# Kernel optimization log

Hardware: AMD Instinct MI355X
Metric: run time of the kernel (lower is better)

## Reference

```python
import jax, jax.numpy as jnp
import numpy as np

V, T_BLOCK, D, H, L, HS = 32000, 1024, 1024, 16, 6, 64
B, T = 4, 1024
EPS = 1e-5


def setup_inputs() -> dict:
    key = jax.random.key(0)
    ks = jax.random.split(key, 12)
    s = 0.02  # init std, matches _init_weights
    return {
        'input_tokens': jax.random.randint(ks[0], (B, T), 0, V),
        'tok_emb': jax.random.normal(ks[1], (V, D), jnp.float32) * s,
        'pos_emb': jax.random.normal(ks[2], (T_BLOCK, D), jnp.float32) * s,
        'Wq': jax.random.normal(ks[3], (L, H, D, HS), jnp.float32) * s,
        'Wk': jax.random.normal(ks[4], (L, H, D, HS), jnp.float32) * s,
        'Wv': jax.random.normal(ks[5], (L, H, D, HS), jnp.float32) * s,
        'Wo': jax.random.normal(ks[6], (L, D, D), jnp.float32) * s,
        'bo': jnp.zeros((L, D), jnp.float32),
        'ln1_g': jnp.ones((L, D), jnp.float32),
        'ln1_b': jnp.zeros((L, D), jnp.float32),
        'ln2_g': jnp.ones((L, D), jnp.float32),
        'ln2_b': jnp.zeros((L, D), jnp.float32),
        'W1': jax.random.normal(ks[7], (L, D, 4 * D), jnp.float32) * s,
        'b1': jnp.zeros((L, 4 * D), jnp.float32),
        'W2': jax.random.normal(ks[8], (L, 4 * D, D), jnp.float32) * s,
        'b2': jnp.zeros((L, D), jnp.float32),
        'lnf_g': jnp.ones((D,), jnp.float32),
        'lnf_b': jnp.zeros((D,), jnp.float32),
        'W_out': jax.random.normal(ks[9], (D, V), jnp.float32) * s,
        'b_out': jnp.zeros((V,), jnp.float32),
    }


def _layer_norm(x, g, b):
    mu = jnp.mean(x, axis=-1, keepdims=True)
    var = jnp.mean(jnp.square(x - mu), axis=-1, keepdims=True)
    return (x - mu) * jax.lax.rsqrt(var + EPS) * g + b


def _attn(x, Wq, Wk, Wv, Wo, bo, causal_mask):
    # x: [B,T,D]; Wq/Wk/Wv: [H,D,hs] (per-head linears, bias=False)
    q = jnp.einsum('btd,hds->bhts', x, Wq)
    k = jnp.einsum('btd,hds->bhts', x, Wk)
    v = jnp.einsum('btd,hds->bhts', x, Wv)
    scores = jnp.einsum('bhts,bhus->bhtu', q, k) * (HS ** -0.5)
    scores = jnp.where(causal_mask, scores, -jnp.inf)
    w = jax.nn.softmax(scores, axis=-1)  # dropout=0.0 -> identity
    o = jnp.einsum('bhtu,bhus->bhts', w, v)
    # concat heads in order, then projection
    o = o.transpose(0, 2, 1, 3).reshape(x.shape[0], x.shape[1], H * HS)
    return o @ Wo + bo


def reference(input_tokens, tok_emb, pos_emb, Wq, Wk, Wv, Wo, bo,
              ln1_g, ln1_b, ln2_g, ln2_b, W1, b1, W2, b2,
              lnf_g, lnf_b, W_out, b_out):
    Bc, Tc = input_tokens.shape
    x = tok_emb[input_tokens] + pos_emb[:Tc]  # [B,T,D]
    mask = jnp.tril(jnp.ones((Tc, Tc), bool))[None, None]  # [1,1,T,T]
    for l in range(L):
        x = x + _attn(_layer_norm(x, ln1_g[l], ln1_b[l]),
                      Wq[l], Wk[l], Wv[l], Wo[l], bo[l], mask)
        h = _layer_norm(x, ln2_g[l], ln2_b[l])
        x = x + jax.nn.relu(h @ W1[l] + b1[l]) @ W2[l] + b2[l]
    x = _layer_norm(x, lnf_g, lnf_b)
    logits = x @ W_out + b_out  # [B,T,V]
    return logits
```

## Files before the change

### kernel.cpp

```cpp
#include <hip/hip_runtime.h>
#include <hip/hip_bf16.h>

#define HS 64
#define NH 16
#define DMODEL 1024
#define SEQ 1024
#define NB 4
#define NL 6
#define VOCAB 32000
#define EPS_LN 1e-5f

static constexpr int ROWS = NB * SEQ;

typedef float f32x4 __attribute__((ext_vector_type(4)));
typedef short bf16x8 __attribute__((ext_vector_type(8)));
typedef unsigned short u16x8 __attribute__((ext_vector_type(8)));
typedef unsigned short u16x4 __attribute__((ext_vector_type(4)));

__device__ __forceinline__ unsigned short f2b(float f) {
  __hip_bfloat16 h = __float2bfloat16(f);
  return *reinterpret_cast<unsigned short*>(&h);
}
__device__ __forceinline__ void gload_lds16(const void* g, void* l) {
  __builtin_amdgcn_global_load_lds(
      (const __attribute__((address_space(1))) void*)g,
      (__attribute__((address_space(3))) void*)l, 16, 0, 0);
}
#define MFMA16 __builtin_amdgcn_mfma_f32_16x16x32_bf16

__global__ __launch_bounds__(256) void embed_kernel(
    const int* __restrict__ tokens, const float* __restrict__ tok_emb,
    const float* __restrict__ pos_emb, float* __restrict__ x) {
  int row = blockIdx.x;
  int t = row & (SEQ - 1);
  int tok = tokens[row];
  int d = threadIdx.x * 4;
  float4 te = *(const float4*)(tok_emb + (size_t)tok * DMODEL + d);
  float4 pe = *(const float4*)(pos_emb + (size_t)t * DMODEL + d);
  te.x += pe.x; te.y += pe.y; te.z += pe.z; te.w += pe.w;
  *(float4*)(x + (size_t)row * DMODEL + d) = te;
}

__global__ __launch_bounds__(256) void ln_kernel(
    const float* __restrict__ in, unsigned short* __restrict__ outp,
    const float* __restrict__ g, const float* __restrict__ b) {
  int row = blockIdx.x;
  int tid = threadIdx.x;
  const float* xr = in + (size_t)row * DMODEL;
  float4 v4 = *(const float4*)(xr + tid * 4);
  float s = v4.x + v4.y + v4.z + v4.w;
  float s2 = v4.x * v4.x + v4.y * v4.y + v4.z * v4.z + v4.w * v4.w;
#pragma unroll
  for (int off = 32; off > 0; off >>= 1) {
    s  += __shfl_down(s, off, 64);
    s2 += __shfl_down(s2, off, 64);
  }
  __shared__ float red[8];
  __shared__ float stats[2];
  int wv = tid >> 6, lane = tid & 63;
  if (lane == 0) { red[wv] = s; red[4 + wv] = s2; }
  __syncthreads();
  if (tid == 0) {
    float ts = red[0] + red[1] + red[2] + red[3];
    float ts2 = red[4] + red[5] + red[6] + red[7];
    float mu = ts * (1.0f / DMODEL);
    float var = ts2 * (1.0f / DMODEL) - mu * mu;
    stats[0] = mu;
    stats[1] = rsqrtf(var + EPS_LN);
  }
  __syncthreads();
  float mu = stats[0], rstd = stats[1];
  float4 g4 = *(const float4*)(g + tid * 4);
  float4 b4 = *(const float4*)(b + tid * 4);
  u16x4 o;
  o[0] = f2b((v4.x - mu) * rstd * g4.x + b4.x);
  o[1] = f2b((v4.y - mu) * rstd * g4.y + b4.y);
  o[2] = f2b((v4.z - mu) * rstd * g4.z + b4.z);
  o[3] = f2b((v4.w - mu) * rstd * g4.w + b4.w);
  *(u16x4*)(outp + (size_t)row * DMODEL + tid * 4) = o;
}

__global__ __launch_bounds__(256) void transconv(
    const float* __restrict__ in, unsigned short* __restrict__ outp, int K, int N) {
  __shared__ float tile[32][33];
  size_t zoff = (size_t)blockIdx.z * K * N;
  in += zoff;
  outp += zoff;
  int n0 = blockIdx.x * 32, k0 = blockIdx.y * 32;
  int tx = threadIdx.x & 31, ty = threadIdx.x >> 5;
#pragma unroll
  for (int i = 0; i < 4; ++i)
    tile[ty + i * 8][tx] = in[(size_t)(k0 + ty + i * 8) * N + n0 + tx];
  __syncthreads();
#pragma unroll
  for (int i = 0; i < 4; ++i)
    outp[(size_t)(n0 + ty + i * 8) * K + k0 + tx] = f2b(tile[tx][ty + i * 8]);
}

__global__ __launch_bounds__(256) void qkv_transconv(
    const float* __restrict__ Wq, const float* __restrict__ Wk,
    const float* __restrict__ Wv, unsigned short* __restrict__ outp) {
  __shared__ float tile[32][33];
  int z = blockIdx.z;
  int l = z / 48;
  int r = z % 48;
  int which = r >> 4, h = r & 15;
  const float* W = (which == 0 ? Wq : which == 1 ? Wk : Wv) +
                   ((size_t)l * NH + h) * DMODEL * HS;
  int d0 = blockIdx.y * 32, s0 = blockIdx.x * 32;
  int tx = threadIdx.x & 31, ty = threadIdx.x >> 5;
#pragma unroll
  for (int i = 0; i < 4; ++i)
    tile[ty + i * 8][tx] = W[(size_t)(d0 + ty + i * 8) * HS + s0 + tx];
  __syncthreads();
  unsigned short* ob = outp + ((size_t)l * 3072 + which * 1024 + h * 64) * DMODEL;
#pragma unroll
  for (int i = 0; i < 4; ++i)
    ob[(size_t)(s0 + ty + i * 8) * DMODEL + d0 + tx] = f2b(tile[tx][ty + i * 8]);
}

#define EPI_LOGITS 0
#define EPI_RES 1
#define EPI_RELU 2
#define EPI_QKV 3

template <int EPI, int BM_>
__global__ __launch_bounds__(512, 2) void mmX(
    const unsigned short* __restrict__ A, const unsigned short* __restrict__ Bt,
    const float* __restrict__ bias, const float* __restrict__ res,
    float* __restrict__ outf, unsigned short* __restrict__ ob0,
    unsigned short* __restrict__ ob1, unsigned short* __restrict__ ob2,
    int M, int N, int K) {
  constexpr int NA = BM_ / 64;
  constexpr int AP = BM_ / 128;
  constexpr int MFRAG = BM_ / 32;
  __shared__ __align__(16) unsigned short LDS[2][(BM_ + 256) * 64];
  const int tid = threadIdx.x;
  const int lane = tid & 63, w = tid >> 6;
  const int wm2 = w >> 2, wn4 = w & 3;
  const int l15 = lane & 15, l4 = lane >> 4;

  const int nM = M / BM_, nN = N >> 8;
  const int nwg = nM * nN;
  int bid = blockIdx.x;
  int wg = (bid & 7) * (nwg >> 3) + (bid >> 3);
  int mb = wg % nM, nb = wg / nM;
  const int m0 = mb * BM_, n0 = nb * 256;

  const int srow = tid >> 3;
  const int scolb = (tid & 7) * 16;
  const int swst = (srow & 7) << 4;
  const char* aS = (const char*)A + ((size_t)(m0 + srow) * K) * 2 + (scolb ^ swst);
  const char* bS = (const char*)Bt + ((size_t)(n0 + srow) * K) * 2 + (scolb ^ swst);
  const size_t rstep = (size_t)64 * K * 2;

  const int kb0 = l4 * 16;
  const int swz = (l15 & 7) << 4;

  const int NT = K >> 6;
  f32x4 acc[MFRAG][4] = {};
  bf16x8 bv[4][2], avA[AP][2], avB[AP][2];

#define STAGEX(tt)                                                          \
  {                                                                         \
    unsigned short* ad = &LDS[(tt) & 1][0] + (size_t)tid * 8;               \
    unsigned short* bd = &LDS[(tt) & 1][BM_ * 64] + (size_t)tid * 8;        \
    size_t ko = (size_t)(tt) * 128;                                         \
    _Pragma("unroll")                                                       \
    for (int j = 0; j < NA; ++j) gload_lds16(aS + ko + j * rstep, ad + j * 4096); \
    _Pragma("unroll")                                                       \
    for (int j = 0; j < 4; ++j) gload_lds16(bS + ko + j * rstep, bd + j * 4096);  \
  }

#define READA(dst, p)                                                       \
  _Pragma("unroll")                                                         \
  for (int mm = 0; mm < AP; ++mm)                                           \
  _Pragma("unroll")                                                         \
    for (int ks = 0; ks < 2; ++ks)                                          \
      dst[mm][ks] = *(const bf16x8*)(ab + (AP * (p) + mm) * 2048 +          \
                                     ((kb0 + 64 * ks) ^ swz));

#define GROUP(src, p)                                                       \
  __builtin_amdgcn_s_setprio(1);                                            \
  _Pragma("unroll")                                                         \
  for (int ks = 0; ks < 2; ++ks)                                            \
  _Pragma("unroll")                                                         \
    for (int mm = 0; mm < AP; ++mm)                                         \
    _Pragma("unroll")                                                       \
      for (int ni = 0; ni < 4; ++ni)                                        \
        acc[AP * (p) + mm][ni] =                                            \
            MFMA16(src[mm][ks], bv[ni][ks], acc[AP * (p) + mm][ni], 0, 0, 0);\
  __builtin_amdgcn_s_setprio(0);

  STAGEX(0)
  STAGEX(1)

  for (int t = 0; t < NT; ++t) {
    if (t < NT - 1) {
      if constexpr (BM_ == 256) asm volatile("s_waitcnt vmcnt(8)" ::: "memory");
      else                      asm volatile("s_waitcnt vmcnt(6)" ::: "memory");
    } else {
      asm volatile("s_waitcnt vmcnt(0)" ::: "memory");
    }
    __builtin_amdgcn_s_barrier();
    __builtin_amdgcn_sched_barrier(0);
    const char* ab = (const char*)&LDS[t & 1][0] +
                     (size_t)(wm2 * (BM_ / 2) + l15) * 128;
    const char* bb = (const char*)&LDS[t & 1][BM_ * 64] +
                     (size_t)(wn4 * 64 + l15) * 128;
#pragma unroll
    for (int ni = 0; ni < 4; ++ni)
#pragma unroll
      for (int ks = 0; ks < 2; ++ks)
        bv[ni][ks] = *(const bf16x8*)(bb + ni * 2048 + ((kb0 + 64 * ks) ^ swz));
    READA(avA, 0)
    READA(avB, 1)
    GROUP(avA, 0)
    READA(avA, 2)
    GROUP(avB, 1)
    READA(avB, 3)
    GROUP(avA, 2)
    asm volatile("s_waitcnt lgkmcnt(0)" ::: "memory");
    __builtin_amdgcn_sched_barrier(0);
    __builtin_amdgcn_s_barrier();
    __builtin_amdgcn_sched_barrier(0);
    if (t + 2 < NT) STAGEX(t + 2)
    GROUP(avB, 3)
  }
#undef STAGEX
#undef READA
#undef GROUP

  int rbase = m0 + wm2 * (BM_ / 2) + (l4 << 2);
  int cbase = n0 + wn4 * 64 + l15;
#pragma unroll
  for (int ni = 0; ni < 4; ++ni) {
    int col = cbase + ni * 16;
    float bvv = 0.f;
    if (EPI != EPI_QKV) bvv = bias[col];
    if (EPI == EPI_QKV) {
      int which = col >> 10;
      int c2 = col & 1023;
      int h = c2 >> 6, s = c2 & 63;
#pragma unroll
      for (int mi = 0; mi < MFRAG; ++mi) {
        f32x4 a4 = acc[mi][ni];
        int row0 = rbase + mi * 16;
        int bb2 = row0 >> 10, t0 = row0 & 1023;
        if (which == 2) {
          u16x4 pk;
          pk[0] = f2b(a4[0]); pk[1] = f2b(a4[1]); pk[2] = f2b(a4[2]); pk[3] = f2b(a4[3]);
          *(u16x4*)(ob2 + ((((size_t)bb2 * NH + h) * HS) + s) * SEQ + t0) = pk;
        } else {
          unsigned short* dst = (which == 0) ? ob0 : ob1;
#pragma unroll
          for (int r = 0; r < 4; ++r)
            dst[((((size_t)bb2 * NH) + h) * SEQ + t0 + r) * HS + s] = f2b(a4[r]);
        }
      }
    } else {
#pragma unroll
      for (int mi = 0; mi < MFRAG; ++mi) {
        f32x4 a4 = acc[mi][ni];
#pragma unroll
        for (int r = 0; r < 4; ++r) {
          int rowg = rbase + mi * 16 + r;
          size_t off = (size_t)rowg * N + col;
          float v = a4[r] + bvv;
          if (EPI == EPI_RES) outf[off] = v + res[off];
          else if (EPI == EPI_LOGITS) outf[off] = v;
          else if (EPI == EPI_RELU) ob0[off] = f2b(fmaxf(v, 0.f));
        }
      }
    }
  }
}

__global__ __launch_bounds__(256) void attn_mfma(
    const unsigned short* __restrict__ q, const unsigned short* __restrict__ k,
    const unsigned short* __restrict__ vt, unsigned short* __restrict__ outp) {
  __shared__ __align__(16) unsigned short S[8192];
  unsigned short* Ks = S;
  unsigned short* Vs = S + 4096;
  int qt = blockIdx.x, bh = blockIdx.y;
  int tid = threadIdx.x;
  int lane = tid & 63, w = tid >> 6;
  int l15 = lane & 15, l4 = lane >> 4;

  const unsigned short* qb = q + (size_t)bh * SEQ * HS;
  const unsigned short* kb = k + (size_t)bh * SEQ * HS;
  const unsigned short* vb = vt + (size_t)bh * HS * SEQ;

  int q_l = w * 16 + l15;
  int q_g = qt * 64 + q_l;
  bf16x8 qf[2];
  qf[0] = *(const bf16x8*)(qb + (size_t)q_g * HS + l4 * 8);
  qf[1] = *(const bf16x8*)(qb + (size_t)q_g * HS + l4 * 8 + 32);

  int i0 = tid, i1 = tid + 256;
  int kOff0 = (i0 >> 7) * 16 * HS + (i0 & 15) * HS + ((i0 >> 4) & 7) * 8;
  int kOff1 = (i1 >> 7) * 16 * HS + (i1 & 15) * HS + ((i1 >> 4) & 7) * 8;
  int vOff0 = ((i0 >> 7) * 16 + (i0 & 15)) * SEQ + ((i0 >> 4) & 7) * 8;
  int vOff1 = ((i1 >> 7) * 16 + (i1 & 15)) * SEQ + ((i1 >> 4) & 7) * 8;

  f32x4 o[4] = {};
  float mrun = -1e30f, lrun = 0.f;
  int baseLane = 32 * (l4 & 1) + l15;
  bool hi_t = (l4 >> 1) != 0;

  for (int kt = 0; kt <= qt; ++kt) {
    __syncthreads();
    const unsigned short* ksrc = kb + (size_t)kt * 64 * HS;
    gload_lds16(ksrc + kOff0, Ks + (size_t)i0 * 8);
    gload_lds16(ksrc + kOff1, Ks + (size_t)i1 * 8);
    gload_lds16(vb + vOff0 + kt * 64, Vs + (size_t)i0 * 8);
    gload_lds16(vb + vOff1 + kt * 64, Vs + (size_t)i1 * 8);
    __syncthreads();

    f32x4 s[4];
#pragma unroll
    for (int t = 0; t < 4; ++t) {
      bf16x8 kf0 = *(const bf16x8*)(Ks + ((size_t)(t * 8 + l4) * 16 + l15) * 8);
      bf16x8 kf1 = *(const bf16x8*)(Ks + ((size_t)(t * 8 + l4 + 4) * 16 + l15) * 8);
      s[t] = (f32x4){0.f, 0.f, 0.f, 0.f};
      s[t] = MFMA16(kf0, qf[0], s[t], 0, 0, 0);
      s[t] = MFMA16(kf1, qf[1], s[t], 0, 0, 0);
    }

    bool diag = (kt == qt);
    int keybase = kt * 64 + 4 * l4;
    float mx = -1e30f;
#pragma unroll
    for (int t = 0; t < 4; ++t)
#pragma unroll
      for (int r = 0; r < 4; ++r) {
        float sv = s[t][r] * 0.125f;
        if (diag && (keybase + 16 * t + r) > q_g) sv = -1e30f;
        s[t][r] = sv;
        mx = fmaxf(mx, sv);
      }
    mx = fmaxf(mx, __shfl_xor(mx, 16, 64));
    mx = fmaxf(mx, __shfl_xor(mx, 32, 64));
    float mnew = fmaxf(mrun, mx);
    float sc = __expf(mrun - mnew);
    float ps = 0.f;
    float p[4][4];
#pragma unroll
    for (int t = 0; t < 4; ++t)
#pragma unroll
      for (int r = 0; r < 4; ++r) {
        float e = __expf(s[t][r] - mnew);
        p[t][r] = e;
        ps += e;
      }
    ps += __shfl_xor(ps, 16, 64);
    ps += __shfl_xor(ps, 32, 64);
    lrun = lrun * sc + ps;
    mrun = mnew;
#pragma unroll
    for (int t2 = 0; t2 < 4; ++t2)
#pragma unroll
      for (int r = 0; r < 4; ++r) o[t2][r] *= sc;

    int pd[4][2];
#pragma unroll
    for (int t = 0; t < 4; ++t)
#pragma unroll
      for (int h = 0; h < 2; ++h)
        pd[t][h] = (int)f2b(p[t][2 * h]) | ((int)f2b(p[t][2 * h + 1]) << 16);

#pragma unroll
    for (int kk = 0; kk < 2; ++kk) {
      int a0 = __shfl(pd[2 * kk][0], baseLane, 64);
      int b0 = __shfl(pd[2 * kk + 1][0], baseLane, 64);
      int a1 = __shfl(pd[2 * kk][1], baseLane, 64);
      int b1 = __shfl(pd[2 * kk + 1][1], baseLane, 64);
      int a2 = __shfl(pd[2 * kk][0], baseLane + 16, 64);
      int b2 = __shfl(pd[2 * kk + 1][0], baseLane + 16, 64);
      int a3 = __shfl(pd[2 * kk][1], baseLane + 16, 64);
      int b3 = __shfl(pd[2 * kk + 1][1], baseLane + 16, 64);
      union { int4 i4; bf16x8 v; } yu;
      yu.i4.x = hi_t ? b0 : a0;
      yu.i4.y = hi_t ? b1 : a1;
      yu.i4.z = hi_t ? b2 : a2;
      yu.i4.w = hi_t ? b3 : a3;
#pragma unroll
      for (int t2 = 0; t2 < 4; ++t2) {
        bf16x8 vf = *(const bf16x8*)(Vs + ((size_t)(t2 * 8 + l4 + 4 * kk) * 16 + l15) * 8);
        o[t2] = MFMA16(vf, yu.v, o[t2], 0, 0, 0);
      }
    }
  }

  __syncthreads();
  float inv = 1.0f / lrun;
  unsigned short* Ol = S;
#pragma unroll
  for (int t2 = 0; t2 < 4; ++t2) {
    u16x4 p4;
#pragma unroll
    for (int r = 0; r < 4; ++r) p4[r] = f2b(o[t2][r] * inv);
    *(u16x4*)(Ol + (size_t)q_l * 72 + 16 * t2 + 4 * l4) = p4;
  }
  __syncthreads();
  int row = tid >> 2, hs0 = (tid & 3) * 16;
  int bidx = bh >> 4, h = bh & 15;
  size_t gbase = ((size_t)bidx * SEQ + qt * 64 + row) * DMODEL + h * HS + hs0;
  u16x8 r0 = *(const u16x8*)(Ol + (size_t)row * 72 + hs0);
  u16x8 r1 = *(const u16x8*)(Ol + (size_t)row * 72 + hs0 + 8);
  *(u16x8*)(outp + gbase) = r0;
  *(u16x8*)(outp + gbase + 8) = r1;
}

extern "C" void kernel_launch(void* const* d_in, const int* in_sizes, int n_in,
                              void* d_out, int out_size, void* d_ws, size_t ws_size,
                              hipStream_t stream) {
  const int*   tokens  = (const int*)d_in[0];
  const float* tok_emb = (const float*)d_in[1];
  const float* pos_emb = (const float*)d_in[2];
  const float* Wq      = (const float*)d_in[3];
  const float* Wk      = (const float*)d_in[4];
  const float* Wv      = (const float*)d_in[5];
  const float* Wo      = (const float*)d_in[6];
  const float* bo      = (const float*)d_in[7];
  const float* ln1_g   = (const float*)d_in[8];
  const float* ln1_b   = (const float*)d_in[9];
  const float* ln2_g   = (const float*)d_in[10];
  const float* ln2_b   = (const float*)d_in[11];
  const float* W1      = (const float*)d_in[12];
  const float* b1      = (const float*)d_in[13];
  const float* W2      = (const float*)d_in[14];
  const float* b2      = (const float*)d_in[15];
  const float* lnf_g   = (const float*)d_in[16];
  const float* lnf_b   = (const float*)d_in[17];
  const float* W_out   = (const float*)d_in[18];
  const float* b_out   = (const float*)d_in[19];
  float* logits = (float*)d_out;

  char* p = (char*)d_ws;
  float* x = (float*)p;            p += (size_t)ROWS * DMODEL * 4;
  unsigned short* hb = (unsigned short*)p;  p += (size_t)ROWS * DMODEL * 2;
  unsigned short* qb = (unsigned short*)p;  p += (size_t)ROWS * DMODEL * 2;
  unsigned short* kb = (unsigned short*)p;  p += (size_t)ROWS * DMODEL * 2;
  unsigned short* vtb = (unsigned short*)p; p += (size_t)ROWS * DMODEL * 2;
  unsigned short* att = (unsigned short*)p; p += (size_t)ROWS * DMODEL * 2;
  unsigned short* hid = (unsigned short*)p; p += (size_t)ROWS * 4 * DMODEL * 2;
  unsigned short* qkvt = (unsigned short*)p; p += (size_t)NL * 3 * DMODEL * DMODEL * 2;
  unsigned short* wot = (unsigned short*)p;  p += (size_t)NL * DMODEL * DMODEL * 2;
  unsigned short* w1t = (unsigned short*)p;  p += (size_t)NL * 4 * DMODEL * DMODEL * 2;
  unsigned short* w2t = (unsigned short*)p;  p += (size_t)NL * 4 * DMODEL * DMODEL * 2;
  unsigned short* woutt = (unsigned short*)p; p += (size_t)VOCAB * DMODEL * 2;

  transconv<<<dim3(32, 32, NL), 256, 0, stream>>>(Wo, wot, DMODEL, DMODEL);
  transconv<<<dim3(128, 32, NL), 256, 0, stream>>>(W1, w1t, DMODEL, 4 * DMODEL);
  transconv<<<dim3(32, 128, NL), 256, 0, stream>>>(W2, w2t, 4 * DMODEL, DMODEL);
  transconv<<<dim3(1000, 32, 1), 256, 0, stream>>>(W_out, woutt, DMODEL, VOCAB);
  qkv_transconv<<<dim3(2, 32, NL * 48), 256, 0, stream>>>(Wq, Wk, Wv, qkvt);

  embed_kernel<<<ROWS, 256, 0, stream>>>(tokens, tok_emb, pos_emb, x);

  for (int l = 0; l < NL; ++l) {
    ln_kernel<<<ROWS, 256, 0, stream>>>(x, hb, ln1_g + l * DMODEL, ln1_b + l * DMODEL);
    mmX<EPI_QKV, 256><<<192, 512, 0, stream>>>(
        hb, qkvt + (size_t)l * 3 * DMODEL * DMODEL, nullptr, nullptr,
        nullptr, qb, kb, vtb, ROWS, 3 * DMODEL, DMODEL);
    attn_mfma<<<dim3(SEQ / 64, NB * NH), 256, 0, stream>>>(qb, kb, vtb, att);
    mmX<EPI_RES, 128><<<128, 512, 0, stream>>>(
        att, wot + (size_t)l * DMODEL * DMODEL, bo + l * DMODEL, x,
        x, nullptr, nullptr, nullptr, ROWS, DMODEL, DMODEL);
    ln_kernel<<<ROWS, 256, 0, stream>>>(x, hb, ln2_g + l * DMODEL, ln2_b + l * DMODEL);
    mmX<EPI_RELU, 256><<<256, 512, 0, stream>>>(
        hb, w1t + (size_t)l * 4 * DMODEL * DMODEL, b1 + (size_t)l * 4 * DMODEL, nullptr,
        nullptr, hid, nullptr, nullptr, ROWS, 4 * DMODEL, DMODEL);
    mmX<EPI_RES, 128><<<128, 512, 0, stream>>>(
        hid, w2t + (size_t)l * 4 * DMODEL * DMODEL, b2 + l * DMODEL, x,
        x, nullptr, nullptr, nullptr, ROWS, DMODEL, 4 * DMODEL);
  }

  ln_kernel<<<ROWS, 256, 0, stream>>>(x, hb, lnf_g, lnf_b);
  mmX<EPI_LOGITS, 256><<<2000, 512, 0, stream>>>(
      hb, woutt, b_out, nullptr, logits, nullptr, nullptr, nullptr,
      ROWS, VOCAB, DMODEL);
}
```

Before: 1.942 ms.

## Vectorize weight transposes, stage logits via LDS, double-buffer attention with lazy rescale

The transpose kernels now handle 64x32 tiles and write eight bf16 values per thread as one 16-byte store, replacing scattered 2-byte stores. The logits GEMM epilogue stages each accumulator half through LDS so it can issue coalesced nontemporal float4 stores to the large logits buffer. The attention kernel double-buffers K/V tiles so the next tile loads while the current one computes, and uses exp2 with a prescaled constant. It also skips the online-softmax rescale unless the running max grows past a threshold. These changes add LDS use and sync points in the GEMM epilogue, and the lazy rescale lets intermediate values grow up to 2^8 before renormalizing.

```diff
diff --git a/kernel.cpp b/kernel.cpp
--- a/kernel.cpp
+++ b/kernel.cpp
@@ -27,6 +27,7 @@
       (__attribute__((address_space(3))) void*)l, 16, 0, 0);
 }
 #define MFMA16 __builtin_amdgcn_mfma_f32_16x16x32_bf16
+#define EXP2F __builtin_amdgcn_exp2f
 
 __global__ __launch_bounds__(256) void embed_kernel(
     const int* __restrict__ tokens, const float* __restrict__ tok_emb,
@@ -82,41 +83,47 @@
 
 __global__ __launch_bounds__(256) void transconv(
     const float* __restrict__ in, unsigned short* __restrict__ outp, int K, int N) {
-  __shared__ float tile[32][33];
+  __shared__ float tile[64][33];
   size_t zoff = (size_t)blockIdx.z * K * N;
   in += zoff;
   outp += zoff;
-  int n0 = blockIdx.x * 32, k0 = blockIdx.y * 32;
+  int n0 = blockIdx.x * 32, k0 = blockIdx.y * 64;
   int tx = threadIdx.x & 31, ty = threadIdx.x >> 5;
 #pragma unroll
-  for (int i = 0; i < 4; ++i)
+  for (int i = 0; i < 8; ++i)
     tile[ty + i * 8][tx] = in[(size_t)(k0 + ty + i * 8) * N + n0 + tx];
   __syncthreads();
-#pragma unroll
-  for (int i = 0; i < 4; ++i)
-    outp[(size_t)(n0 + ty + i * 8) * K + k0 + tx] = f2b(tile[tx][ty + i * 8]);
+  int n = threadIdx.x >> 3;
+  int kq = (threadIdx.x & 7) * 8;
+  u16x8 o8;
+#pragma unroll
+  for (int j = 0; j < 8; ++j) o8[j] = f2b(tile[kq + j][n]);
+  *(u16x8*)(outp + (size_t)(n0 + n) * K + k0 + kq) = o8;
 }
 
 __global__ __launch_bounds__(256) void qkv_transconv(
     const float* __restrict__ Wq, const float* __restrict__ Wk,
     const float* __restrict__ Wv, unsigned short* __restrict__ outp) {
-  __shared__ float tile[32][33];
+  __shared__ float tile[64][33];
   int z = blockIdx.z;
   int l = z / 48;
   int r = z % 48;
   int which = r >> 4, h = r & 15;
   const float* W = (which == 0 ? Wq : which == 1 ? Wk : Wv) +
                    ((size_t)l * NH + h) * DMODEL * HS;
-  int d0 = blockIdx.y * 32, s0 = blockIdx.x * 32;
+  int s0 = blockIdx.x * 32, d0 = blockIdx.y * 64;
   int tx = threadIdx.x & 31, ty = threadIdx.x >> 5;
 #pragma unroll
-  for (int i = 0; i < 4; ++i)
+  for (int i = 0; i < 8; ++i)
     tile[ty + i * 8][tx] = W[(size_t)(d0 + ty + i * 8) * HS + s0 + tx];
   __syncthreads();
   unsigned short* ob = outp + ((size_t)l * 3072 + which * 1024 + h * 64) * DMODEL;
-#pragma unroll
-  for (int i = 0; i < 4; ++i)
-    ob[(size_t)(s0 + ty + i * 8) * DMODEL + d0 + tx] = f2b(tile[tx][ty + i * 8]);
+  int n = threadIdx.x >> 3;
+  int kq = (threadIdx.x & 7) * 8;
+  u16x8 o8;
+#pragma unroll
+  for (int j = 0; j < 8; ++j) o8[j] = f2b(tile[kq + j][n]);
+  *(u16x8*)(ob + (size_t)(s0 + n) * DMODEL + d0 + kq) = o8;
 }
 
 #define EPI_LOGITS 0
@@ -233,43 +240,75 @@
 
   int rbase = m0 + wm2 * (BM_ / 2) + (l4 << 2);
   int cbase = n0 + wn4 * 64 + l15;
-#pragma unroll
-  for (int ni = 0; ni < 4; ++ni) {
-    int col = cbase + ni * 16;
-    float bvv = 0.f;
-    if (EPI != EPI_QKV) bvv = bias[col];
-    if (EPI == EPI_QKV) {
-      int which = col >> 10;
-      int c2 = col & 1023;
-      int h = c2 >> 6, s = c2 & 63;
-#pragma unroll
-      for (int mi = 0; mi < MFRAG; ++mi) {
-        f32x4 a4 = acc[mi][ni];
-        int row0 = rbase + mi * 16;
-        int bb2 = row0 >> 10, t0 = row0 & 1023;
-        if (which == 2) {
-          u16x4 pk;
-          pk[0] = f2b(a4[0]); pk[1] = f2b(a4[1]); pk[2] = f2b(a4[2]); pk[3] = f2b(a4[3]);
-          *(u16x4*)(ob2 + ((((size_t)bb2 * NH + h) * HS) + s) * SEQ + t0) = pk;
-        } else {
-          unsigned short* dst = (which == 0) ? ob0 : ob1;
-#pragma unroll
-          for (int r = 0; r < 4; ++r)
-            dst[((((size_t)bb2 * NH) + h) * SEQ + t0 + r) * HS + s] = f2b(a4[r]);
+
+  if constexpr (EPI == EPI_LOGITS) {
+    float* fl = (float*)&LDS[0][0];
+#pragma unroll
+    for (int half = 0; half < 2; ++half) {
+      __syncthreads();
+      if (wm2 == half) {
+#pragma unroll
+        for (int ni = 0; ni < 4; ++ni) {
+          float bvv = bias[cbase + ni * 16];
+          int cl = wn4 * 64 + l15 + ni * 16;
+#pragma unroll
+          for (int mi = 0; mi < MFRAG; ++mi) {
+            int rl = mi * 16 + (l4 << 2);
+#pragma unroll
+            for (int r = 0; r < 4; ++r)
+              fl[(rl + r) * 256 + cl] = acc[mi][ni][r] + bvv;
+          }
         }
       }
-    } else {
-#pragma unroll
-      for (int mi = 0; mi < MFRAG; ++mi) {
-        f32x4 a4 = acc[mi][ni];
-#pragma unroll
-        for (int r = 0; r < 4; ++r) {
-          int rowg = rbase + mi * 16 + r;
-          size_t off = (size_t)rowg * N + col;
-          float v = a4[r] + bvv;
-          if (EPI == EPI_RES) outf[off] = v + res[off];
-          else if (EPI == EPI_LOGITS) outf[off] = v;
-          else if (EPI == EPI_RELU) ob0[off] = f2b(fmaxf(v, 0.f));
+      __syncthreads();
+#pragma unroll
+      for (int j = 0; j < 16; ++j) {
+        int idx = j * 512 + tid;
+        int rl = idx >> 6;
+        int cc = (idx & 63) << 2;
+        f32x4 v4 = *(const f32x4*)&fl[rl * 256 + cc];
+        float* gp = outf + (size_t)(m0 + half * 128 + rl) * N + n0 + cc;
+        __builtin_nontemporal_store(v4, (f32x4*)gp);
+      }
+    }
+  } else {
+#pragma unroll
+    for (int ni = 0; ni < 4; ++ni) {
+      int col = cbase + ni * 16;
+      float bvv = 0.f;
+      if (EPI != EPI_QKV) bvv = bias[col];
+      if (EPI == EPI_QKV) {
+        int which = col >> 10;
+        int c2 = col & 1023;
+        int h = c2 >> 6, s = c2 & 63;
+#pragma unroll
+        for (int mi = 0; mi < MFRAG; ++mi) {
+          f32x4 a4 = acc[mi][ni];
+          int row0 = rbase + mi * 16;
+          int bb2 = row0 >> 10, t0 = row0 & 1023;
+          if (which == 2) {
+            u16x4 pk;
+            pk[0] = f2b(a4[0]); pk[1] = f2b(a4[1]); pk[2] = f2b(a4[2]); pk[3] = f2b(a4[3]);
+            *(u16x4*)(ob2 + ((((size_t)bb2 * NH + h) * HS) + s) * SEQ + t0) = pk;
+          } else {
+            unsigned short* dst = (which == 0) ? ob0 : ob1;
+#pragma unroll
+            for (int r = 0; r < 4; ++r)
+              dst[((((size_t)bb2 * NH) + h) * SEQ + t0 + r) * HS + s] = f2b(a4[r]);
+          }
+        }
+      } else {
+#pragma unroll
+        for (int mi = 0; mi < MFRAG; ++mi) {
+          f32x4 a4 = acc[mi][ni];
+#pragma unroll
+          for (int r = 0; r < 4; ++r) {
+            int rowg = rbase + mi * 16 + r;
+            size_t off = (size_t)rowg * N + col;
+            float v = a4[r] + bvv;
+            if (EPI == EPI_RES) outf[off] = v + res[off];
+            else if (EPI == EPI_RELU) ob0[off] = f2b(fmaxf(v, 0.f));
+          }
         }
       }
     }
@@ -279,9 +318,9 @@
 __global__ __launch_bounds__(256) void attn_mfma(
     const unsigned short* __restrict__ q, const unsigned short* __restrict__ k,
     const unsigned short* __restrict__ vt, unsigned short* __restrict__ outp) {
-  __shared__ __align__(16) unsigned short S[8192];
+  __shared__ __align__(16) unsigned short S[16384];
   unsigned short* Ks = S;
-  unsigned short* Vs = S + 4096;
+  unsigned short* Vs = S + 8192;
   int qt = blockIdx.x, bh = blockIdx.y;
   int tid = threadIdx.x;
   int lane = tid & 63, w = tid >> 6;
@@ -303,64 +342,82 @@
   int vOff0 = ((i0 >> 7) * 16 + (i0 & 15)) * SEQ + ((i0 >> 4) & 7) * 8;
   int vOff1 = ((i1 >> 7) * 16 + (i1 & 15)) * SEQ + ((i1 >> 4) & 7) * 8;
 
+#define ASTAGE(tt)                                                           \
+  {                                                                          \
+    int bsel = ((tt) & 1) * 4096;                                            \
+    const unsigned short* ksrc = kb + (size_t)(tt) * 64 * HS;                \
+    gload_lds16(ksrc + kOff0, Ks + bsel + (size_t)i0 * 8);                   \
+    gload_lds16(ksrc + kOff1, Ks + bsel + (size_t)i1 * 8);                   \
+    gload_lds16(vb + vOff0 + (tt) * 64, Vs + bsel + (size_t)i0 * 8);         \
+    gload_lds16(vb + vOff1 + (tt) * 64, Vs + bsel + (size_t)i1 * 8);         \
+  }
+
   f32x4 o[4] = {};
-  float mrun = -1e30f, lrun = 0.f;
+  float mrun = -3e38f, lrun = 0.f;
   int baseLane = 32 * (l4 & 1) + l15;
   bool hi_t = (l4 >> 1) != 0;
+  const float CSC = 0.125f * 1.44269504f;
+  const float THR = 8.0f / CSC;
+
+  ASTAGE(0)
 
   for (int kt = 0; kt <= qt; ++kt) {
-    __syncthreads();
-    const unsigned short* ksrc = kb + (size_t)kt * 64 * HS;
-    gload_lds16(ksrc + kOff0, Ks + (size_t)i0 * 8);
-    gload_lds16(ksrc + kOff1, Ks + (size_t)i1 * 8);
-    gload_lds16(vb + vOff0 + kt * 64, Vs + (size_t)i0 * 8);
-    gload_lds16(vb + vOff1 + kt * 64, Vs + (size_t)i1 * 8);
-    __syncthreads();
+    asm volatile("s_waitcnt vmcnt(0)" ::: "memory");
+    __builtin_amdgcn_s_barrier();
+    __builtin_amdgcn_sched_barrier(0);
+    if (kt < qt) ASTAGE(kt + 1)
+    const unsigned short* Kb = Ks + (kt & 1) * 4096;
+    const unsigned short* Vb = Vs + (kt & 1) * 4096;
 
     f32x4 s[4];
 #pragma unroll
     for (int t = 0; t < 4; ++t) {
-      bf16x8 kf0 = *(const bf16x8*)(Ks + ((size_t)(t * 8 + l4) * 16 + l15) * 8);
-      bf16x8 kf1 = *(const bf16x8*)(Ks + ((size_t)(t * 8 + l4 + 4) * 16 + l15) * 8);
+      bf16x8 kf0 = *(const bf16x8*)(Kb + ((size_t)(t * 8 + l4) * 16 + l15) * 8);
+      bf16x8 kf1 = *(const bf16x8*)(Kb + ((size_t)(t * 8 + l4 + 4) * 16 + l15) * 8);
       s[t] = (f32x4){0.f, 0.f, 0.f, 0.f};
       s[t] = MFMA16(kf0, qf[0], s[t], 0, 0, 0);
       s[t] = MFMA16(kf1, qf[1], s[t], 0, 0, 0);
     }
 
-    bool diag = (kt == qt);
-    int keybase = kt * 64 + 4 * l4;
-    float mx = -1e30f;
+    if (kt == qt) {
+      int keybase = kt * 64 + 4 * l4;
+#pragma unroll
+      for (int t = 0; t < 4; ++t)
+#pragma unroll
+        for (int r = 0; r < 4; ++r)
+          if (keybase + 16 * t + r > q_g) s[t][r] = -3e38f;
+    }
+    float mx = -3e38f;
 #pragma unroll
     for (int t = 0; t < 4; ++t)
 #pragma unroll
-      for (int r = 0; r < 4; ++r) {
-        float sv = s[t][r] * 0.125f;
-        if (diag && (keybase + 16 * t + r) > q_g) sv = -1e30f;
-        s[t][r] = sv;
-        mx = fmaxf(mx, sv);
-      }
+      for (int r = 0; r < 4; ++r) mx = fmaxf(mx, s[t][r]);
     mx = fmaxf(mx, __shfl_xor(mx, 16, 64));
     mx = fmaxf(mx, __shfl_xor(mx, 32, 64));
-    float mnew = fmaxf(mrun, mx);
-    float sc = __expf(mrun - mnew);
+    if (!__all(mx - mrun <= THR)) {
+      float mnew = fmaxf(mrun, mx);
+      float sc = EXP2F((mrun - mnew) * CSC);
+      lrun *= sc;
+#pragma unroll
+      for (int t2 = 0; t2 < 4; ++t2)
+#pragma unroll
+        for (int r = 0; r < 4; ++r) o[t2][r] *= sc;
+      mrun = mnew;
+    }
+    float mc = mrun * CSC;
     float ps = 0.f;
     float p[4][4];
 #pragma unroll
     for (int t = 0; t < 4; ++t)
 #pragma unroll
       for (int r = 0; r < 4; ++r) {
-        float e = __expf(s[t][r] - mnew);
+        float e = EXP2F(__builtin_fmaf(s[t][r], CSC, -mc));
         p[t][r] = e;
         ps += e;
       }
     ps += __shfl_xor(ps, 16, 64);
     ps += __shfl_xor(ps, 32, 64);
-    lrun = lrun * sc + ps;
-    mrun = mnew;
-#pragma unroll
-    for (int t2 = 0; t2 < 4; ++t2)
-#pragma unroll
-      for (int r = 0; r < 4; ++r) o[t2][r] *= sc;
+    lrun += ps;
 
     int pd[4][2];
 #pragma unroll
@@ -386,11 +443,12 @@
       yu.i4.w = hi_t ? b3 : a3;
 #pragma unroll
       for (int t2 = 0; t2 < 4; ++t2) {
-        bf16x8 vf = *(const bf16x8*)(Vs + ((size_t)(t2 * 8 + l4 + 4 * kk) * 16 + l15) * 8);
+        bf16x8 vf = *(const bf16x8*)(Vb + ((size_t)(t2 * 8 + l4 + 4 * kk) * 16 + l15) * 8);
         o[t2] = MFMA16(vf, yu.v, o[t2], 0, 0, 0);
       }
     }
   }
+#undef ASTAGE
 
   __syncthreads();
   float inv = 1.0f / lrun;
@@ -451,11 +509,11 @@
   unsigned short* w2t = (unsigned short*)p;  p += (size_t)NL * 4 * DMODEL * DMODEL * 2;
   unsigned short* woutt = (unsigned short*)p; p += (size_t)VOCAB * DMODEL * 2;
 
-  transconv<<<dim3(32, 32, NL), 256, 0, stream>>>(Wo, wot, DMODEL, DMODEL);
-  transconv<<<dim3(128, 32, NL), 256, 0, stream>>>(W1, w1t, DMODEL, 4 * DMODEL);
-  transconv<<<dim3(32, 128, NL), 256, 0, stream>>>(W2, w2t, 4 * DMODEL, DMODEL);
-  transconv<<<dim3(1000, 32, 1), 256, 0, stream>>>(W_out, woutt, DMODEL, VOCAB);
-  qkv_transconv<<<dim3(2, 32, NL * 48), 256, 0, stream>>>(Wq, Wk, Wv, qkvt);
+  transconv<<<dim3(32, 16, NL), 256, 0, stream>>>(Wo, wot, DMODEL, DMODEL);
+  transconv<<<dim3(128, 16, NL), 256, 0, stream>>>(W1, w1t, DMODEL, 4 * DMODEL);
+  transconv<<<dim3(32, 64, NL), 256, 0, stream>>>(W2, w2t, 4 * DMODEL, DMODEL);
+  transconv<<<dim3(1000, 16, 1), 256, 0, stream>>>(W_out, woutt, DMODEL, VOCAB);
+  qkv_transconv<<<dim3(2, 16, NL * 48), 256, 0, stream>>>(Wq, Wk, Wv, qkvt);
 
   embed_kernel<<<ROWS, 256, 0, stream>>>(tokens, tok_emb, pos_emb, x);
 
```

Result: faster. 1.828 ms (-5.9%).
